# Optimization experiments

Hardware: AMD Instinct MI355X
Metric: run time of the kernel (lower is better)

Reference implementation:

```python
import jax, jax.numpy as jnp
import numpy as np

V, E, DY, DZ, H, B, T = 32000, 100, 200, 500, 700, 32, 128

def _glorot(key, shape):
    fan_in, fan_out = shape[0], shape[-1]
    lim = np.sqrt(6.0 / (fan_in + fan_out)).astype(np.float32)
    return jax.random.uniform(key, shape, jnp.float32, -lim, lim)

def setup_inputs() -> dict:
    key = jax.random.key(0)
    ks = jax.random.split(key, 16)
    labels = jax.random.randint(ks[0], (B,), 0, 2).astype(jnp.float32)
    z = jax.random.normal(ks[1], (B, DZ), jnp.float32)
    dec_inputs = jax.random.randint(ks[2], (B, T), 0, V)
    # tf.nn.dropout(rate=0.5): keep w.p. 0.5, scale kept by 1/0.5 -> mask in {0, 2}
    dropout_mask = (jax.random.uniform(ks[3], (B, T, H)) < 0.5).astype(jnp.float32) * 2.0
    emb = jax.random.normal(ks[4], (V, E), jnp.float32) * 0.05
    W1 = _glorot(ks[5], (1, DY)); b1 = jnp.zeros((DY,), jnp.float32)
    gru1_k = _glorot(ks[6], (E, 3 * H))
    gru1_rk = _glorot(ks[7], (H, 3 * H))
    gru1_b = jnp.zeros((2, 3 * H), jnp.float32)
    proj_W = _glorot(ks[8], (H, V)); proj_b = jnp.zeros((V,), jnp.float32)
    gru3_k = _glorot(ks[9], (E, 3 * H))
    gru3_rk = _glorot(ks[10], (H, 3 * H))
    gru3_b = jnp.zeros((2, 3 * H), jnp.float32)
    return {"labels": labels, "z": z, "dec_inputs": dec_inputs, "dropout_mask": dropout_mask,
            "emb": emb, "W1": W1, "b1": b1,
            "gru1_k": gru1_k, "gru1_rk": gru1_rk, "gru1_b": gru1_b,
            "proj_W": proj_W, "proj_b": proj_b,
            "gru3_k": gru3_k, "gru3_rk": gru3_rk, "gru3_b": gru3_b}

def _run_gru(x_seq, h0, k, rk, b):
    # Keras GRU, reset_after=True: bias shape [2, 3H]
    xp = jnp.einsum('bti,ij->btj', x_seq, k) + b[0]  # input projections for all steps
    def step(h, xp_t):
        hp = h @ rk + b[1]
        xz, xr, xh = jnp.split(xp_t, 3, axis=-1)
        hz, hr, hhp = jnp.split(hp, 3, axis=-1)
        zg = jax.nn.sigmoid(xz + hz)
        rg = jax.nn.sigmoid(xr + hr)
        hh = jnp.tanh(xh + rg * hhp)
        hn = zg * h + (1.0 - zg) * hh
        return hn, hn
    hN, ys = jax.lax.scan(step, h0, jnp.swapaxes(xp, 0, 1))
    return jnp.swapaxes(ys, 0, 1), hN  # [B,T,H], [B,H]

def reference(labels, z, dec_inputs, dropout_mask, emb, W1, b1,
              gru1_k, gru1_rk, gru1_b, proj_W, proj_b,
              gru3_k, gru3_rk, gru3_b):
    x = emb[dec_inputs]                          # [B,T,E]
    lab = labels.reshape(-1, 1)                  # [B,1]
    h_ori = jnp.concatenate([lab @ W1 + b1, z], axis=1)        # [B,H]
    h_tsf = jnp.concatenate([(1.0 - lab) @ W1 + b1, z], axis=1)
    g_outputs, _ = _run_gru(x, h_ori, gru1_k, gru1_rk, gru1_b)  # [B,T,H]
    g = (g_outputs * dropout_mask).reshape(-1, g_outputs.shape[-1])
    g_logits = g @ proj_W + proj_b               # [B*T, V]
    # soft_h_tsf computed in original but unused by the return (pruned by TF/XLA alike)
    _soft, _second = _run_gru(x, h_tsf, gru3_k, gru3_rk, gru3_b)
    return g_logits
```

## Files before the change

kernel.cpp:

```cpp
#include <hip/hip_runtime.h>
#include <hip/hip_bf16.h>

#define B_   32
#define T_   128
#define H_   700
#define E_   100
#define G3   2100
#define V_   32000
#define DY_  200
#define DZ_  500
#define KP   704
#define NBLK 88
#define JW   8
#define FSTR 16
#define BT   4096
#define NTILE (32 * 250)

typedef __attribute__((ext_vector_type(8))) short bf16x8;
typedef __attribute__((ext_vector_type(4))) float f32x4;
typedef __attribute__((ext_vector_type(4))) unsigned u32x4;

__device__ __forceinline__ unsigned ld_flag(const unsigned* p) {
    return __hip_atomic_load(p, __ATOMIC_RELAXED, __HIP_MEMORY_SCOPE_AGENT);
}
__device__ __forceinline__ void st_flag(unsigned* p, unsigned v) {
    __hip_atomic_store(p, v, __ATOMIC_RELAXED, __HIP_MEMORY_SCOPE_AGENT);
}
__device__ __forceinline__ void split_bf(float v, short& hi, short& lo) {
    __hip_bfloat16 h = __float2bfloat16(v);
    float r = v - __bfloat162float(h);
    __hip_bfloat16 l = __float2bfloat16(r);
    hi = *reinterpret_cast<short*>(&h);
    lo = *reinterpret_cast<short*>(&l);
}

#define GLDS16(g, l) __builtin_amdgcn_global_load_lds(                            \
        (const __attribute__((address_space(1))) unsigned int*)(g),               \
        (__attribute__((address_space(3))) unsigned int*)(l), 16, 0, 0)

__global__ __launch_bounds__(256)
void wconv_kernel(const float* __restrict__ W, __hip_bfloat16* __restrict__ Wb) {
    __shared__ float tile[32][33];
    const int n0 = blockIdx.x * 32, k0 = blockIdx.y * 32;
    const int tx = threadIdx.x, ty = threadIdx.y;
    #pragma unroll
    for (int i = 0; i < 4; ++i) {
        int k = k0 + ty + 8 * i;
        float v = (k < H_) ? W[(size_t)k * V_ + n0 + tx] : 0.0f;
        tile[ty + 8 * i][tx] = v;
    }
    __syncthreads();
    #pragma unroll
    for (int i = 0; i < 4; ++i) {
        int nn = ty + 8 * i;
        Wb[(size_t)(n0 + nn) * KP + k0 + tx] = __float2bfloat16(tile[tx][nn]);
    }
}

__global__ __launch_bounds__(256)
void xpt_gemm(const int* __restrict__ di, const float* __restrict__ emb,
              const float* __restrict__ gk, const float* __restrict__ gb,
              float* __restrict__ xpt) {
    __shared__ int di_l[64];
    __shared__ unsigned short Bhi[64][136], Blo[64][136];
    const int tid = threadIdx.x;
    const int c0 = blockIdx.x * 64, n0 = blockIdx.y * 64;
    const int wv = tid >> 6, lane = tid & 63, lr = lane & 15, lkg = lane >> 4;

    if (tid < 64) {
        int tb = n0 + tid;
        di_l[tid] = di[(tb & 31) * T_ + (tb >> 5)];
    }
    __syncthreads();
    for (int e = tid; e < 64 * 128; e += 256) {
        int r = e >> 7, k = e & 127;
        float v = (k < E_) ? emb[(size_t)di_l[r] * E_ + k] : 0.0f;
        short hi, lo; split_bf(v, hi, lo);
        Bhi[r][k] = (unsigned short)hi; Blo[r][k] = (unsigned short)lo;
    }
    __syncthreads();

    bf16x8 ahi[4], alo[4];
    const int crow = c0 + wv * 16 + lr;
    #pragma unroll
    for (int kt = 0; kt < 4; ++kt) {
        #pragma unroll
        for (int i = 0; i < 8; ++i) {
            int k = kt * 32 + lkg * 8 + i;
            float v = (k < E_ && crow < G3) ? gk[(size_t)k * G3 + crow] : 0.0f;
            short hi, lo; split_bf(v, hi, lo);
            ahi[kt][i] = hi; alo[kt][i] = lo;
        }
    }
    f32x4 acc[4];
    #pragma unroll
    for (int n = 0; n < 4; ++n) acc[n] = (f32x4){0.f, 0.f, 0.f, 0.f};
    #pragma unroll
    for (int kt = 0; kt < 4; ++kt) {
        #pragma unroll
        for (int n = 0; n < 4; ++n) {
            bf16x8 bh = *(const bf16x8*)&Bhi[n * 16 + lr][kt * 32 + lkg * 8];
            bf16x8 bl = *(const bf16x8*)&Blo[n * 16 + lr][kt * 32 + lkg * 8];
            acc[n] = __builtin_amdgcn_mfma_f32_16x16x32_bf16(ahi[kt], bh, acc[n], 0, 0, 0);
            acc[n] = __builtin_amdgcn_mfma_f32_16x16x32_bf16(ahi[kt], bl, acc[n], 0, 0, 0);
            acc[n] = __builtin_amdgcn_mfma_f32_16x16x32_bf16(alo[kt], bh, acc[n], 0, 0, 0);
        }
    }
    #pragma unroll
    for (int n = 0; n < 4; ++n)
        #pragma unroll
        for (int r = 0; r < 4; ++r) {
            int cr = c0 + wv * 16 + lkg * 4 + r;
            if (cr < G3)
                xpt[(size_t)cr * BT + n0 + n * 16 + lr] = acc[n][r] + gb[cr];
        }
}

__global__ __launch_bounds__(256, 2)
void mega_kernel(const float* __restrict__ labels, const float* __restrict__ zin,
                 const float* __restrict__ W1, const float* __restrict__ b1,
                 const float* __restrict__ xpt, const float* __restrict__ mask,
                 const float* __restrict__ rk, const float* __restrict__ gb,
                 unsigned short* __restrict__ hb, unsigned short* __restrict__ g_out,
                 unsigned* __restrict__ flags, int* __restrict__ wcnt,
                 const __hip_bfloat16* __restrict__ Bw, const float* __restrict__ bias,
                 float* __restrict__ C) {
    __shared__ float part2[4 * 2 * 16 * 33];
    __shared__ float xbuf[24 * 32];
    __shared__ alignas(16) short smhi[32 * 8], smlo[32 * 8], smg[32 * 8];
    __shared__ alignas(16) unsigned short As[128 * 64];
    __shared__ alignas(16) unsigned short Bs[128 * 64];
    __shared__ int s_idx;

    const int tid = threadIdx.x;
    const int blk = blockIdx.x;

    if (blk < NBLK) {
        __builtin_amdgcn_s_setprio(1);
        const int j0 = blk * JW;
        const int wv = tid >> 6, lane = tid & 63, lr = lane & 15, lkg = lane >> 4;
        const int ktb = (wv < 2) ? wv * 6 : 12 + (wv - 2) * 5;
        const int tn  = (wv < 2) ? 6 : 5;

        bf16x8 bhi[2][6], blo[2][6];
        #pragma unroll
        for (int n = 0; n < 2; ++n)
            #pragma unroll
            for (int t = 0; t < 6; ++t) {
                bf16x8 h8, l8;
                int c = n * 16 + lr;
                int gate = c >> 3, jl = c & 7, j = j0 + jl;
                #pragma unroll
                for (int i = 0; i < 8; ++i) {
                    int k = (ktb + t) * 32 + lkg * 8 + i;
                    float v = (t < tn && c < 24 && j < H_ && k < H_)
                                ? rk[(size_t)k * G3 + gate * H_ + j] : 0.0f;
                    short hi, lo; split_bf(v, hi, lo);
                    h8[i] = hi; l8[i] = lo;
                }
                bhi[n][t] = h8; blo[n][t] = l8;
            }

        const int ob = tid & 31, ojl = tid >> 5, oj = j0 + ojl;
        float hold = 0.f, bz = 0.f, brr = 0.f, bh = 0.f;
        if (oj < H_) {
            bz  = gb[G3 + oj];
            brr = gb[G3 + H_ + oj];
            bh  = gb[G3 + 2 * H_ + oj];
            hold = (oj < DY_) ? labels[ob] * W1[oj] + b1[oj] : zin[ob * DZ_ + (oj - DY_)];
        }
        {
            short hi, lo; split_bf(hold, hi, lo);
            smhi[ob * 8 + ojl] = hi; smlo[ob * 8 + ojl] = lo;
        }
        __syncthreads();
        if (tid < 64) {
            int pl = tid >> 5, q = tid & 31;
            u32x4 d = ((const u32x4*)(pl ? smlo : smhi))[q];
            unsigned short* dst = hb + (size_t)blk * 512 + pl * 256 + q * 8;
            asm volatile("global_store_dwordx4 %0, %1, off sc0 sc1" :: "v"(dst), "v"(d) : "memory");
        }
        asm volatile("s_waitcnt vmcnt(0)" ::: "memory");
        __syncthreads();
        if (tid == 0) st_flag(&flags[blk * FSTR], 1u);

        union FragU { u32x4 u; bf16x8 v; };
        struct Chunk { u32x4 a0, l0, a1, l1; };

#define LOADC(T, Cc) do {                                                         \
        const unsigned short* rb = hb + (size_t)cur * 45056                       \
                                     + (size_t)((ktb + (T)) * 4 + lkg) * 512;     \
        asm volatile("global_load_dwordx4 %0, %1, off sc0 sc1"                    \
                     : "=v"((Cc).a0) : "v"(rb + lr * 8) : "memory");              \
        asm volatile("global_load_dwordx4 %0, %1, off sc0 sc1"                    \
                     : "=v"((Cc).l0) : "v"(rb + 256 + lr * 8) : "memory");        \
        asm volatile("global_load_dwordx4 %0, %1, off sc0 sc1"                    \
                     : "=v"((Cc).a1) : "v"(rb + 128 + lr * 8) : "memory");        \
        asm volatile("global_load_dwordx4 %0, %1, off sc0 sc1"                    \
                     : "=v"((Cc).l1) : "v"(rb + 384 + lr * 8) : "memory");        \
    } while (0)
#define PROCC(T, Cc) do {                                                         \
        FragU fa0, fl0, fa1, fl1;                                                 \
        fa0.u = (Cc).a0; fl0.u = (Cc).l0; fa1.u = (Cc).a1; fl1.u = (Cc).l1;       \
        _Pragma("unroll")                                                         \
        for (int n = 0; n < 2; ++n) {                                             \
            acc[0][n] = __builtin_amdgcn_mfma_f32_16x16x32_bf16(fa0.v, bhi[n][T], acc[0][n], 0, 0, 0); \
            acc[0][n] = __builtin_amdgcn_mfma_f32_16x16x32_bf16(fa0.v, blo[n][T], acc[0][n], 0, 0, 0); \
            acc[0][n] = __builtin_amdgcn_mfma_f32_16x16x32_bf16(fl0.v, bhi[n][T], acc[0][n], 0, 0, 0); \
            acc[1][n] = __builtin_amdgcn_mfma_f32_16x16x32_bf16(fa1.v, bhi[n][T], acc[1][n], 0, 0, 0); \
            acc[1][n] = __builtin_amdgcn_mfma_f32_16x16x32_bf16(fa1.v, blo[n][T], acc[1][n], 0, 0, 0); \
            acc[1][n] = __builtin_amdgcn_mfma_f32_16x16x32_bf16(fl1.v, bhi[n][T], acc[1][n], 0, 0, 0); \
        }                                                                         \
    } while (0)
#define VWAIT(N) do { asm volatile("s_waitcnt vmcnt(" #N ")" ::: "memory");       \
                      __builtin_amdgcn_sched_barrier(0); } while (0)

        for (int step = 0; step < T_; ++step) {
            const int cur = step & 1, nxt = cur ^ 1;

            #pragma unroll
            for (int it = 0; it < 3; ++it) {
                int e = tid + it * 256;
                int row = e >> 5, b = e & 31;
                int gate = row >> 3, jl = row & 7, j = j0 + jl;
                xbuf[e] = (j < H_) ? xpt[(size_t)(gate * H_ + j) * BT + step * 32 + b] : 0.f;
            }
            float mvr = (oj < H_) ? mask[(size_t)(ob * T_ + step) * H_ + oj] : 0.f;

            if (tid < NBLK) {
                while (ld_flag(&flags[tid * FSTR]) < (unsigned)(step + 1))
                    __builtin_amdgcn_s_sleep(1);
            }
            __syncthreads();
            VWAIT(0);

            f32x4 acc[2][2];
            #pragma unroll
            for (int m = 0; m < 2; ++m)
                #pragma unroll
                for (int n = 0; n < 2; ++n) acc[m][n] = (f32x4){0.f, 0.f, 0.f, 0.f};
            Chunk c0, c1, c2;
            LOADC(0, c0); LOADC(1, c1); LOADC(2, c2);
            VWAIT(8); PROCC(0, c0); LOADC(3, c0);
            VWAIT(8); PROCC(1, c1); LOADC(4, c1);
            VWAIT(8); PROCC(2, c2); LOADC(5, c2);
            VWAIT(8); PROCC(3, c0);
            VWAIT(4); PROCC(4, c1);
            VWAIT(0); PROCC(5, c2);

            #pragma unroll
            for (int m = 0; m < 2; ++m)
                #pragma unroll
                for (int n = 0; n < 2; ++n)
                    #pragma unroll
                    for (int r = 0; r < 4; ++r)
                        part2[((wv * 2 + m) * 16 + lkg * 4 + r) * 33 + n * 16 + lr] = acc[m][n][r];
            __syncthreads();

            {
                int m = ob >> 4, row = ob & 15;
                float hp0 = bz, hp1 = brr, hp2 = bh;
                #pragma unroll
                for (int w = 0; w < 4; ++w) {
                    int base = ((w * 2 + m) * 16 + row) * 33;
                    hp0 += part2[base + ojl];
                    hp1 += part2[base + 8 + ojl];
                    hp2 += part2[base + 16 + ojl];
                }
                float hn = 0.f, outf = 0.f;
                if (oj < H_) {
                    float xz = xbuf[(0 * 8 + ojl) * 32 + ob];
                    float xr = xbuf[(1 * 8 + ojl) * 32 + ob];
                    float xh = xbuf[(2 * 8 + ojl) * 32 + ob];
                    float zg = 1.0f / (1.0f + expf(-(xz + hp0)));
                    float rg = 1.0f / (1.0f + expf(-(xr + hp1)));
                    float hh = tanhf(xh + rg * hp2);
                    hn = zg * hold + (1.0f - zg) * hh;
                    outf = hn * mvr;
                }
                hold = hn;
                __hip_bfloat16 ov = __float2bfloat16(outf);
                smg[ob * 8 + ojl] = *(short*)&ov;
                short hi, lo; split_bf(hn, hi, lo);
                smhi[ob * 8 + ojl] = hi; smlo[ob * 8 + ojl] = lo;
            }
            __syncthreads();
            if (tid < 64) {
                int pl = tid >> 5, q = tid & 31;
                u32x4 d = ((const u32x4*)(pl ? smlo : smhi))[q];
                unsigned short* dst = hb + (size_t)nxt * 45056 + (size_t)blk * 512 + pl * 256 + q * 8;
                asm volatile("global_store_dwordx4 %0, %1, off sc0 sc1" :: "v"(dst), "v"(d) : "memory");
            } else if (tid < 96) {
                int b = tid - 64;
                u32x4 d = ((const u32x4*)smg)[b];
                unsigned short* gp = g_out + (size_t)(step * 32 + b) * KP + j0;
                asm volatile("global_store_dwordx4 %0, %1, off sc0 sc1" :: "v"(gp), "v"(d) : "memory");
            }
            asm volatile("s_waitcnt vmcnt(0)" ::: "memory");
            __syncthreads();
            if (tid == 0) st_flag(&flags[blk * FSTR], (unsigned)(step + 2));
        }
        __builtin_amdgcn_s_setprio(0);
#undef LOADC
#undef PROCC
#undef VWAIT
    }

    {
        const __hip_bfloat16* Ag = (const __hip_bfloat16*)g_out;
        const int lane = tid & 63, w = tid >> 6;
        const int wm = w >> 1, wn = w & 1;
        const int lr = lane & 15, lkg = lane >> 4;
        const int srl = lane >> 3, scol = (lane & 7) * 8;
        unsigned satisfied = 0;
        for (;;) {
            __syncthreads();
            if (tid == 0)
                s_idx = __hip_atomic_fetch_add(wcnt, 1, __ATOMIC_RELAXED, __HIP_MEMORY_SCOPE_AGENT);
            __syncthreads();
            const int idx = s_idx;
            if (idx >= NTILE) break;
            const int m = idx / 250, bn = idx - m * 250;
            const unsigned want = (unsigned)(4 * m + 5);
            if (want > satisfied) {
                if (tid < NBLK) {
                    while (ld_flag(&flags[tid * FSTR]) < want) __builtin_amdgcn_s_sleep(64);
                }
                satisfied = want;
            }
            __syncthreads();
            const int rowbase = m * 128, colbase = bn * 128;

            f32x4 acc[4][4];
            #pragma unroll
            for (int i = 0; i < 4; ++i)
                #pragma unroll
                for (int j = 0; j < 4; ++j) acc[i][j] = (f32x4){0.f, 0.f, 0.f, 0.f};

            for (int kt = 0; kt < 11; ++kt) {
                const int k0 = kt * 64;
                __syncthreads();
                #pragma unroll
                for (int i = 0; i < 4; ++i) {
                    const int r0 = w * 32 + i * 8;
                    GLDS16(&Ag[(size_t)(rowbase + r0 + srl) * KP + k0 + scol], &As[r0 * 64]);
                    GLDS16(&Bw[(size_t)(colbase + r0 + srl) * KP + k0 + scol], &Bs[r0 * 64]);
                }
                __syncthreads();
                #pragma unroll
                for (int ks = 0; ks < 2; ++ks) {
                    bf16x8 af[4], bf[4];
                    #pragma unroll
                    for (int i = 0; i < 4; ++i)
                        af[i] = *(const bf16x8*)&As[(wm * 64 + i * 16 + lr) * 64 + ks * 32 + lkg * 8];
                    #pragma unroll
                    for (int j = 0; j < 4; ++j)
                        bf[j] = *(const bf16x8*)&Bs[(wn * 64 + j * 16 + lr) * 64 + ks * 32 + lkg * 8];
                    #pragma unroll
                    for (int i = 0; i < 4; ++i)
                        #pragma unroll
                        for (int j = 0; j < 4; ++j)
                            acc[i][j] = __builtin_amdgcn_mfma_f32_16x16x32_bf16(af[i], bf[j], acc[i][j], 0, 0, 0);
                }
            }

            float bv[4];
            #pragma unroll
            for (int j = 0; j < 4; ++j) bv[j] = bias[colbase + wn * 64 + j * 16 + lr];
            #pragma unroll
            for (int i = 0; i < 4; ++i) {
                int gr0 = rowbase + wm * 64 + i * 16 + lkg * 4;
                #pragma unroll
                for (int j = 0; j < 4; ++j) {
                    int gcol = colbase + wn * 64 + j * 16 + lr;
                    #pragma unroll
                    for (int r = 0; r < 4; ++r) {
                        int gr = gr0 + r;
                        int orow = (gr & 31) * T_ + (gr >> 5);
                        float val = acc[i][j][r] + bv[j];
                        float* cp = &C[(size_t)orow * V_ + gcol];
                        asm volatile("global_store_dword %0, %1, off nt"
                                     :: "v"(cp), "v"(val) : "memory");
                    }
                }
            }
        }
    }
}

extern "C" void kernel_launch(void* const* d_in, const int* in_sizes, int n_in,
                              void* d_out, int out_size, void* d_ws, size_t ws_size,
                              hipStream_t stream) {
    const float* labels = (const float*)d_in[0];
    const float* z      = (const float*)d_in[1];
    const int*   di     = (const int*)d_in[2];
    const float* mask   = (const float*)d_in[3];
    const float* emb    = (const float*)d_in[4];
    const float* W1     = (const float*)d_in[5];
    const float* b1     = (const float*)d_in[6];
    const float* g1k    = (const float*)d_in[7];
    const float* g1rk   = (const float*)d_in[8];
    const float* g1b    = (const float*)d_in[9];
    const float* pW     = (const float*)d_in[10];
    const float* pb     = (const float*)d_in[11];

    char* ws = (char*)d_ws;
    unsigned short* g     = (unsigned short*)ws;
    __hip_bfloat16* Wb    = (__hip_bfloat16*)(ws + 5767168);
    float*          xpt   = (float*)(ws + 50823168);
    unsigned short* hb    = (unsigned short*)(ws + 85229568);
    unsigned*       flags = (unsigned*)(ws + 85409792);
    int*            wcnt  = (int*)(ws + 85415424);

    hipMemsetAsync(flags, 0, 5632 + 64, stream);

    xpt_gemm<<<dim3(33, 64), 256, 0, stream>>>(di, emb, g1k, g1b, xpt);
    wconv_kernel<<<dim3(1000, 22), dim3(32, 8), 0, stream>>>(pW, Wb);

    mega_kernel<<<dim3(512), 256, 0, stream>>>(labels, z, W1, b1, xpt, mask,
                                               g1rk, g1b, hb, g, flags, wcnt,
                                               Wb, pb, (float*)d_out);
}
```

Before: 668.4 us.

## Fold weight bf16 conversion into mega kernel, overlap with GRU; widen GEMM tile

After: 674.8 us. Within noise of the previous version (+1.0%).

```diff
diff --git a/kernel.cpp b/kernel.cpp
--- a/kernel.cpp
+++ b/kernel.cpp
@@ -14,7 +14,8 @@
 #define JW   8
 #define FSTR 16
 #define BT   4096
-#define NTILE (32 * 250)
+#define NWORK 424
+#define NTILE 4000
 
 typedef __attribute__((ext_vector_type(8))) short bf16x8;
 typedef __attribute__((ext_vector_type(4))) float f32x4;
@@ -37,25 +38,6 @@
 #define GLDS16(g, l) __builtin_amdgcn_global_load_lds(                            \
         (const __attribute__((address_space(1))) unsigned int*)(g),               \
         (__attribute__((address_space(3))) unsigned int*)(l), 16, 0, 0)
-
-__global__ __launch_bounds__(256)
-void wconv_kernel(const float* __restrict__ W, __hip_bfloat16* __restrict__ Wb) {
-    __shared__ float tile[32][33];
-    const int n0 = blockIdx.x * 32, k0 = blockIdx.y * 32;
-    const int tx = threadIdx.x, ty = threadIdx.y;
-    #pragma unroll
-    for (int i = 0; i < 4; ++i) {
-        int k = k0 + ty + 8 * i;
-        float v = (k < H_) ? W[(size_t)k * V_ + n0 + tx] : 0.0f;
-        tile[ty + 8 * i][tx] = v;
-    }
-    __syncthreads();
-    #pragma unroll
-    for (int i = 0; i < 4; ++i) {
-        int nn = ty + 8 * i;
-        Wb[(size_t)(n0 + nn) * KP + k0 + tx] = __float2bfloat16(tile[tx][nn]);
-    }
-}
 
 __global__ __launch_bounds__(256)
 void xpt_gemm(const int* __restrict__ di, const float* __restrict__ emb,
@@ -122,14 +104,14 @@
                  const float* __restrict__ xpt, const float* __restrict__ mask,
                  const float* __restrict__ rk, const float* __restrict__ gb,
                  unsigned short* __restrict__ hb, unsigned short* __restrict__ g_out,
-                 unsigned* __restrict__ flags, int* __restrict__ wcnt,
-                 const __hip_bfloat16* __restrict__ Bw, const float* __restrict__ bias,
-                 float* __restrict__ C) {
+                 unsigned* __restrict__ flags, unsigned* __restrict__ ctrs,
+                 const float* __restrict__ W, __hip_bfloat16* __restrict__ Wb,
+                 const float* __restrict__ bias, float* __restrict__ C) {
     __shared__ float part2[4 * 2 * 16 * 33];
     __shared__ float xbuf[24 * 32];
     __shared__ alignas(16) short smhi[32 * 8], smlo[32 * 8], smg[32 * 8];
     __shared__ alignas(16) unsigned short As[128 * 64];
-    __shared__ alignas(16) unsigned short Bs[128 * 64];
+    __shared__ alignas(16) unsigned short Bs[256 * 64];
     __shared__ int s_idx;
 
     const int tid = threadIdx.x;
@@ -304,7 +286,43 @@
 #undef LOADC
 #undef PROCC
 #undef VWAIT
-    }
+    } else {
+        float (*wtile)[33] = (float(*)[33])As;
+        const int wi = blk - NBLK;
+        const int tx = tid & 31, ty8 = tid >> 5;
+        for (int tI = wi; tI < 22000; tI += NWORK) {
+            const int n0 = (tI % 1000) * 32, k0 = (tI / 1000) * 32;
+            #pragma unroll
+            for (int i = 0; i < 4; ++i) {
+                int k = k0 + ty8 + 8 * i;
+                wtile[ty8 + 8 * i][tx] = (k < H_) ? W[(size_t)k * V_ + n0 + tx] : 0.0f;
+            }
+            __syncthreads();
+            if (tid < 128) {
+                int ty = tid >> 2, q = tid & 3;
+                u32x4 d;
+                #pragma unroll
+                for (int e = 0; e < 4; ++e) {
+                    __hip_bfloat16 b0 = __float2bfloat16(wtile[q * 8 + 2 * e][ty]);
+                    __hip_bfloat16 b1 = __float2bfloat16(wtile[q * 8 + 2 * e + 1][ty]);
+                    d[e] = (unsigned)*(unsigned short*)&b0
+                         | ((unsigned)*(unsigned short*)&b1 << 16);
+                }
+                unsigned short* wp = (unsigned short*)Wb + (size_t)(n0 + ty) * KP + k0 + q * 8;
+                asm volatile("global_store_dwordx4 %0, %1, off sc0 sc1" :: "v"(wp), "v"(d) : "memory");
+            }
+            __syncthreads();
+        }
+        asm volatile("s_waitcnt vmcnt(0)" ::: "memory");
+        __syncthreads();
+        if (tid == 0)
+            __hip_atomic_fetch_add(&ctrs[16], 1u, __ATOMIC_RELAXED, __HIP_MEMORY_SCOPE_AGENT);
+    }
+
+    if (tid == 0) {
+        while (ld_flag(&ctrs[16]) < (unsigned)NWORK) __builtin_amdgcn_s_sleep(64);
+    }
+    __syncthreads();
 
     {
         const __hip_bfloat16* Ag = (const __hip_bfloat16*)g_out;
@@ -316,11 +334,12 @@
         for (;;) {
             __syncthreads();
             if (tid == 0)
-                s_idx = __hip_atomic_fetch_add(wcnt, 1, __ATOMIC_RELAXED, __HIP_MEMORY_SCOPE_AGENT);
+                s_idx = (int)__hip_atomic_fetch_add((int*)&ctrs[0], 1, __ATOMIC_RELAXED,
+                                                    __HIP_MEMORY_SCOPE_AGENT);
             __syncthreads();
             const int idx = s_idx;
             if (idx >= NTILE) break;
-            const int m = idx / 250, bn = idx - m * 250;
+            const int m = idx / 125, bn = idx - m * 125;
             const unsigned want = (unsigned)(4 * m + 5);
             if (want > satisfied) {
                 if (tid < NBLK) {
@@ -329,13 +348,13 @@
                 satisfied = want;
             }
             __syncthreads();
-            const int rowbase = m * 128, colbase = bn * 128;
-
-            f32x4 acc[4][4];
+            const int rowbase = m * 128, colbase = bn * 256;
+
+            f32x4 acc[4][8];
             #pragma unroll
             for (int i = 0; i < 4; ++i)
                 #pragma unroll
-                for (int j = 0; j < 4; ++j) acc[i][j] = (f32x4){0.f, 0.f, 0.f, 0.f};
+                for (int j = 0; j < 8; ++j) acc[i][j] = (f32x4){0.f, 0.f, 0.f, 0.f};
 
             for (int kt = 0; kt < 11; ++kt) {
                 const int k0 = kt * 64;
@@ -344,35 +363,39 @@
                 for (int i = 0; i < 4; ++i) {
                     const int r0 = w * 32 + i * 8;
                     GLDS16(&Ag[(size_t)(rowbase + r0 + srl) * KP + k0 + scol], &As[r0 * 64]);
-                    GLDS16(&Bw[(size_t)(colbase + r0 + srl) * KP + k0 + scol], &Bs[r0 * 64]);
+                }
+                #pragma unroll
+                for (int i = 0; i < 8; ++i) {
+                    const int r0 = w * 64 + i * 8;
+                    GLDS16(&Wb[(size_t)(colbase + r0 + srl) * KP + k0 + scol], &Bs[r0 * 64]);
                 }
                 __syncthreads();
                 #pragma unroll
                 for (int ks = 0; ks < 2; ++ks) {
-                    bf16x8 af[4], bf[4];
+                    bf16x8 af[4], bf[8];
                     #pragma unroll
                     for (int i = 0; i < 4; ++i)
                         af[i] = *(const bf16x8*)&As[(wm * 64 + i * 16 + lr) * 64 + ks * 32 + lkg * 8];
                     #pragma unroll
-                    for (int j = 0; j < 4; ++j)
-                        bf[j] = *(const bf16x8*)&Bs[(wn * 64 + j * 16 + lr) * 64 + ks * 32 + lkg * 8];
+                    for (int j = 0; j < 8; ++j)
+                        bf[j] = *(const bf16x8*)&Bs[(wn * 128 + j * 16 + lr) * 64 + ks * 32 + lkg * 8];
                     #pragma unroll
                     for (int i = 0; i < 4; ++i)
                         #pragma unroll
-                        for (int j = 0; j < 4; ++j)
+                        for (int j = 0; j < 8; ++j)
                             acc[i][j] = __builtin_amdgcn_mfma_f32_16x16x32_bf16(af[i], bf[j], acc[i][j], 0, 0, 0);
                 }
             }
 
-            float bv[4];
-            #pragma unroll
-            for (int j = 0; j < 4; ++j) bv[j] = bias[colbase + wn * 64 + j * 16 + lr];
+            float bv[8];
+            #pragma unroll
+            for (int j = 0; j < 8; ++j) bv[j] = bias[colbase + wn * 128 + j * 16 + lr];
             #pragma unroll
             for (int i = 0; i < 4; ++i) {
                 int gr0 = rowbase + wm * 64 + i * 16 + lkg * 4;
                 #pragma unroll
-                for (int j = 0; j < 4; ++j) {
-                    int gcol = colbase + wn * 64 + j * 16 + lr;
+                for (int j = 0; j < 8; ++j) {
+                    int gcol = colbase + wn * 128 + j * 16 + lr;
                     #pragma unroll
                     for (int r = 0; r < 4; ++r) {
                         int gr = gr0 + r;
@@ -410,14 +433,13 @@
     float*          xpt   = (float*)(ws + 50823168);
     unsigned short* hb    = (unsigned short*)(ws + 85229568);
     unsigned*       flags = (unsigned*)(ws + 85409792);
-    int*            wcnt  = (int*)(ws + 85415424);
-
-    hipMemsetAsync(flags, 0, 5632 + 64, stream);
+    unsigned*       ctrs  = (unsigned*)(ws + 85415424);
+
+    hipMemsetAsync(flags, 0, 5632 + 128, stream);
 
     xpt_gemm<<<dim3(33, 64), 256, 0, stream>>>(di, emb, g1k, g1b, xpt);
-    wconv_kernel<<<dim3(1000, 22), dim3(32, 8), 0, stream>>>(pW, Wb);
 
     mega_kernel<<<dim3(512), 256, 0, stream>>>(labels, z, W1, b1, xpt, mask,
-                                               g1rk, g1b, hb, g, flags, wcnt,
-                                               Wb, pb, (float*)d_out);
-}
+                                               g1rk, g1b, hb, g, flags, ctrs,
+                                               pW, Wb, pb, (float*)d_out);
+}
```
